# Kernel tuning notes

Measured on AMD Instinct MI355X. Metric: run time of the kernel, lower is better.

## Reference

```python
import jax, jax.numpy as jnp
import numpy as np

EPS = 1e-5

def _layer_norm(x, gamma, beta):
    mu = jnp.mean(x, axis=-1, keepdims=True)
    var = jnp.mean(jnp.square(x - mu), axis=-1, keepdims=True)
    return (x - mu) * jax.lax.rsqrt(var + EPS) * gamma + beta

def setup_inputs() -> dict:
    key = jax.random.key(0)
    ks = jax.random.split(key, 16)
    B, N, E, D = 1024, 64, 1024, 512
    s_e = 1.0 / np.sqrt(E)
    s_d = 1.0 / np.sqrt(D)
    return {
        "role_embeddings": jax.random.normal(ks[0], (B, N, E), jnp.float32),
        "context": jax.random.normal(ks[1], (B, D), jnp.float32),
        "qW": jax.random.uniform(ks[2], (E, E), jnp.float32, -s_e, s_e),
        "qb": jax.random.uniform(ks[3], (E,), jnp.float32, -s_e, s_e),
        "kW": jax.random.uniform(ks[4], (E, D), jnp.float32, -s_d, s_d),
        "kb": jax.random.uniform(ks[5], (E,), jnp.float32, -s_d, s_d),
        "vW": jax.random.uniform(ks[6], (E, D), jnp.float32, -s_d, s_d),
        "vb": jax.random.uniform(ks[7], (E,), jnp.float32, -s_d, s_d),
        "oW": jax.random.uniform(ks[8], (E, E), jnp.float32, -s_e, s_e),
        "ob": jax.random.uniform(ks[9], (E,), jnp.float32, -s_e, s_e),
        "lnq_g": jnp.ones((E,), jnp.float32),
        "lnq_b": jnp.zeros((E,), jnp.float32),
        "lnk_g": jnp.ones((D,), jnp.float32),
        "lnk_b": jnp.zeros((D,), jnp.float32),
    }

def reference(role_embeddings, context, qW, qb, kW, kb, vW, vb, oW, ob, lnq_g, lnq_b, lnk_g, lnk_b):
    E = role_embeddings.shape[-1]
    ctx = context[:, None, :]                                   # [B, 1, D]
    q = _layer_norm(role_embeddings, lnq_g, lnq_b) @ qW.T + qb  # [B, N, E]
    nk = _layer_norm(ctx, lnk_g, lnk_b)                         # [B, 1, D]
    k = nk @ kW.T + kb                                          # [B, 1, E]
    v = nk @ vW.T + vb                                          # [B, 1, E]
    scale = E ** (-0.5)
    scores = jnp.einsum('bne,bke->bnk', q, k) * scale           # [B, N, 1]
    attn = jnp.tanh(scores)
    out = attn * v                                              # broadcast -> [B, N, E]
    return (out + role_embeddings) @ oW.T + ob
```

## Files before the change

kernel.cpp:

```cpp
#include <hip/hip_runtime.h>

#define E_DIM 1024
#define D_DIM 512
#define B_DIM 1024
#define N_SEQ 64
#define M_ROWS (B_DIM * N_SEQ)

typedef __attribute__((ext_vector_type(8))) short bf16x8;
typedef __attribute__((ext_vector_type(4))) float f32x4;
typedef __attribute__((ext_vector_type(8))) unsigned short u16x8;

__device__ __forceinline__ float bf2f(unsigned short b) {
    union { unsigned int u; float f; } v; v.u = ((unsigned int)b) << 16; return v.f;
}
__device__ __forceinline__ unsigned short f2bf(float f) {
    union { float f; unsigned int u; } v; v.f = f;
    unsigned int r = v.u + 0x7FFFu + ((v.u >> 16) & 1u);
    return (unsigned short)(r >> 16);
}
__device__ __forceinline__ bool detect_bf16(const void* det) {
    return *(const unsigned int*)det == 0x3F803F80u;
}
__device__ __forceinline__ void load8(const void* p, size_t idx, bool isbf, float o[8]) {
    if (isbf) {
        const u16x8 v = *(const u16x8*)((const unsigned short*)p + idx);
#pragma unroll
        for (int j = 0; j < 8; j++) o[j] = bf2f(v[j]);
    } else {
        const float4 a = *(const float4*)((const float*)p + idx);
        const float4 b = *(const float4*)((const float*)p + idx + 4);
        o[0]=a.x; o[1]=a.y; o[2]=a.z; o[3]=a.w; o[4]=b.x; o[5]=b.y; o[6]=b.z; o[7]=b.w;
    }
}
__device__ __forceinline__ float load1(const void* p, size_t idx, bool isbf) {
    return isbf ? bf2f(((const unsigned short*)p)[idx]) : ((const float*)p)[idx];
}
__device__ __forceinline__ void gload16(const void* g, void* l) {
    __builtin_amdgcn_global_load_lds((const __attribute__((address_space(1))) void*)g,
                                     (__attribute__((address_space(3))) void*)l, 16, 0, 0);
}

__device__ __forceinline__ void block_reduce_2(float& s, float& s2, float* smem) {
#pragma unroll
    for (int off = 32; off; off >>= 1) {
        s  += __shfl_xor(s,  off, 64);
        s2 += __shfl_xor(s2, off, 64);
    }
    const int wave = threadIdx.x >> 6, lane = threadIdx.x & 63;
    if (lane == 0) { smem[wave * 2] = s; smem[wave * 2 + 1] = s2; }
    __syncthreads();
    s  = smem[0] + smem[2] + smem[4] + smem[6];
    s2 = smem[1] + smem[3] + smem[5] + smem[7];
}
__device__ __forceinline__ void block_reduce_3(float& a, float& b, float& c, float* smem) {
#pragma unroll
    for (int off = 32; off; off >>= 1) {
        a += __shfl_xor(a, off, 64);
        b += __shfl_xor(b, off, 64);
        c += __shfl_xor(c, off, 64);
    }
    const int wave = threadIdx.x >> 6, lane = threadIdx.x & 63;
    if (lane == 0) { smem[wave * 3] = a; smem[wave * 3 + 1] = b; smem[wave * 3 + 2] = c; }
    __syncthreads();
    a = smem[0] + smem[3] + smem[6] + smem[9];
    b = smem[1] + smem[4] + smem[7] + smem[10];
    c = smem[2] + smem[5] + smem[8] + smem[11];
}

__global__ void ctxln_k(const void* __restrict__ ctx, const void* __restrict__ g,
                        const void* __restrict__ bta, const void* __restrict__ det,
                        float* __restrict__ nk) {
    __shared__ float sm[8];
    const bool isbf = detect_bf16(det);
    const size_t base = (size_t)blockIdx.x * D_DIM;
    const int t = threadIdx.x;
    const float x0 = load1(ctx, base + t * 2, isbf);
    const float x1 = load1(ctx, base + t * 2 + 1, isbf);
    float s = x0 + x1, s2 = x0 * x0 + x1 * x1;
    block_reduce_2(s, s2, sm);
    const float m = s * (1.f / D_DIM);
    const float rs = rsqrtf(s2 * (1.f / D_DIM) - m * m + 1e-5f);
    nk[base + t * 2]     = (x0 - m) * rs * load1(g, t * 2, isbf)     + load1(bta, t * 2, isbf);
    nk[base + t * 2 + 1] = (x1 - m) * rs * load1(g, t * 2 + 1, isbf) + load1(bta, t * 2 + 1, isbf);
}

__global__ void transpose_k(const void* __restrict__ Win, const void* __restrict__ det,
                            float* __restrict__ out) {
    __shared__ float tile[32][33];
    const bool isbf = detect_bf16(det);
    const int bx = blockIdx.x * 32, by = blockIdx.y * 32;
    const int tx = threadIdx.x & 31, ty4 = (threadIdx.x >> 5) * 4;
#pragma unroll
    for (int i = 0; i < 4; i++)
        tile[ty4 + i][tx] = load1(Win, (size_t)(by + ty4 + i) * E_DIM + bx + tx, isbf);
    __syncthreads();
#pragma unroll
    for (int i = 0; i < 4; i++)
        out[(size_t)(bx + ty4 + i) * E_DIM + by + tx] = tile[tx][ty4 + i];
}

__global__ void castw_k(const void* __restrict__ Win, const void* __restrict__ det,
                        unsigned short* __restrict__ out, int n) {
    const bool isbf = detect_bf16(det);
    const int i = (blockIdx.x * 256 + threadIdx.x) * 8;
    if (i >= n) return;
    float a8[8];
    load8(Win, (size_t)i, isbf, a8);
    u16x8 h;
#pragma unroll
    for (int j = 0; j < 8; j++) h[j] = f2bf(a8[j]);
    *(u16x8*)(out + i) = h;
}

template <bool FORCEF32, int KDIM>
__launch_bounds__(256)
__global__ void sgemm_k(const float* __restrict__ A, const void* __restrict__ W,
                        const void* __restrict__ bias, float* __restrict__ C,
                        const void* __restrict__ det, int Ncols) {
    __shared__ __align__(16) unsigned short As[64][40];
    __shared__ __align__(16) unsigned short Bs[64][40];
    const bool isbf = FORCEF32 ? false : detect_bf16(det);
    const int tid = threadIdx.x;
    const int tileM = blockIdx.y * 64;
    const int tileN = blockIdx.x * 64;
    const int r = tid >> 2;
    const int cseg = (tid & 3) * 8;
    const int gm = tileM + r;
    const int gn = tileN + r;
    const int lane = tid & 63;
    const int wave = tid >> 6;
    const int quad = lane >> 4;
    const int l16 = lane & 15;

    f32x4 acc[4];
#pragma unroll
    for (int i = 0; i < 4; i++) acc[i] = (f32x4){0.f, 0.f, 0.f, 0.f};

    for (int k0 = 0; k0 < KDIM; k0 += 32) {
        const int gk = k0 + cseg;
        float a8[8], w8[8];
        load8(A, (size_t)gm * KDIM + gk, false, a8);
        load8(W, (size_t)gn * KDIM + gk, isbf, w8);
        __syncthreads();
#pragma unroll
        for (int j = 0; j < 8; j++) {
            As[r][cseg + j] = f2bf(a8[j]);
            Bs[r][cseg + j] = f2bf(w8[j]);
        }
        __syncthreads();
        const bf16x8 a = *(const bf16x8*)&As[wave * 16 + l16][quad * 8];
#pragma unroll
        for (int nt = 0; nt < 4; nt++) {
            const bf16x8 b = *(const bf16x8*)&Bs[nt * 16 + l16][quad * 8];
            acc[nt] = __builtin_amdgcn_mfma_f32_16x16x32_bf16(a, b, acc[nt], 0, 0, 0);
        }
    }
#pragma unroll
    for (int nt = 0; nt < 4; nt++) {
        const int gc = tileN + nt * 16 + l16;
        const float bv = bias ? load1(bias, gc, isbf) : 0.f;
#pragma unroll
        for (int rg = 0; rg < 4; rg++) {
            const int grow = tileM + wave * 16 + quad * 4 + rg;
            C[(size_t)grow * Ncols + gc] = acc[nt][rg] + bv;
        }
    }
}

__global__ void prep_k(const float* __restrict__ kvec, const float* __restrict__ kk,
                       const void* __restrict__ qb, const void* __restrict__ g,
                       const void* __restrict__ bta, const void* __restrict__ det,
                       float* __restrict__ gk, float* __restrict__ S1, float* __restrict__ C0) {
    __shared__ float sm[12];
    const bool isbf = detect_bf16(det);
    const size_t base = (size_t)blockIdx.x * E_DIM;
    const int t = threadIdx.x;
    float c = 0.f, s1 = 0.f, s2 = 0.f;
#pragma unroll
    for (int j = 0; j < 4; j++) {
        const int idx = t * 4 + j;
        const float kv = kvec[base + idx], kkv = kk[base + idx];
        const float gv = load1(g, idx, isbf);
        c  += load1(qb, idx, isbf) * kv;
        s1 += gv * kkv;
        s2 += load1(bta, idx, isbf) * kkv;
        gk[base + idx] = gv * kkv;
    }
    block_reduce_3(c, s1, s2, sm);
    if (t == 0) { S1[blockIdx.x] = s1; C0[blockIdx.x] = s2 + c; }
}

__global__ void rowscore_k(const void* __restrict__ role, const void* __restrict__ det,
                           const float* __restrict__ gk, const float* __restrict__ S1,
                           const float* __restrict__ C0, float* __restrict__ attn) {
    __shared__ float sm[12];
    const bool isbf = detect_bf16(det);
    const size_t m = blockIdx.x;
    const int b = (int)(m >> 6);
    const size_t base = m * E_DIM;
    const int t = threadIdx.x;
    float x[4];
    if (isbf) {
        const uint2 u = *(const uint2*)((const unsigned short*)role + base + t * 4);
        x[0] = bf2f(u.x & 0xFFFF); x[1] = bf2f(u.x >> 16);
        x[2] = bf2f(u.y & 0xFFFF); x[3] = bf2f(u.y >> 16);
    } else {
        const float4 v = *(const float4*)((const float*)role + base + t * 4);
        x[0]=v.x; x[1]=v.y; x[2]=v.z; x[3]=v.w;
    }
    const float4 gv = *(const float4*)(gk + ((size_t)b << 10) + t * 4);
    float s = 0.f, s2 = 0.f, d = 0.f;
    s = x[0]+x[1]+x[2]+x[3];
    s2 = x[0]*x[0]+x[1]*x[1]+x[2]*x[2]+x[3]*x[3];
    d = x[0]*gv.x + x[1]*gv.y + x[2]*gv.z + x[3]*gv.w;
    block_reduce_3(s, s2, d, sm);
    if (t == 0) {
        const float mu = s * (1.f / E_DIM);
        const float rstd = rsqrtf(s2 * (1.f / E_DIM) - mu * mu + 1e-5f);
        const float score = rstd * (d - mu * S1[b]) + C0[b];
        attn[m] = tanhf(score * 0.03125f);
    }
}

__launch_bounds__(256)
__global__ void outgemm_k(const void* __restrict__ role, const unsigned short* __restrict__ oWb,
                          const float* __restrict__ attn, const float* __restrict__ vo,
                          const void* __restrict__ ob, void* __restrict__ out,
                          const void* __restrict__ det) {
    __shared__ __align__(16) unsigned short As[128 * 32];
    __shared__ __align__(16) unsigned short Bs[128 * 32];
    const bool isbf = detect_bf16(det);
    const int tid = threadIdx.x;
    const int wave = tid >> 6, lane = tid & 63;
    const int quad = lane >> 4, l16 = lane & 15;
    const int wm = wave >> 1, wn = wave & 1;

    const int id = blockIdx.x + (blockIdx.y << 3);
    const int sid = (id & 7) * 512 + (id >> 3);
    const int tileN = (sid & 7) * 128;
    const int tileM = (sid >> 3) * 128;

    const int srow = lane >> 2;
    const int scol = (lane & 3) * 8;
    const int ar = tid >> 2;
    const int ac = (tid & 3) * 8;

    f32x4 acc[4][4];
#pragma unroll
    for (int i = 0; i < 4; i++)
#pragma unroll
        for (int j = 0; j < 4; j++) acc[i][j] = (f32x4){0.f, 0.f, 0.f, 0.f};

    const float* rolef = (const float*)role;
    const unsigned short* roleh = (const unsigned short*)role;

    for (int k0 = 0; k0 < E_DIM; k0 += 32) {
        __syncthreads();
#pragma unroll
        for (int c = 0; c < 2; c++) {
            const int cb = c * 4 + wave;
            const unsigned short* gp = oWb + (size_t)(tileN + cb * 16 + srow) * E_DIM + k0 + scol;
            gload16(gp, Bs + cb * 512);
        }
        if (isbf) {
#pragma unroll
            for (int c = 0; c < 2; c++) {
                const int cb = c * 4 + wave;
                const unsigned short* gp = roleh + (size_t)(tileM + cb * 16 + srow) * E_DIM + k0 + scol;
                gload16(gp, As + cb * 512);
            }
        } else {
#pragma unroll
            for (int c = 0; c < 2; c++) {
                const int rr = c * 64 + ar;
                const float* gp = rolef + (size_t)(tileM + rr) * E_DIM + k0 + ac;
                const float4 f0 = ((const float4*)gp)[0];
                const float4 f1 = ((const float4*)gp)[1];
                u16x8 h;
                h[0]=f2bf(f0.x); h[1]=f2bf(f0.y); h[2]=f2bf(f0.z); h[3]=f2bf(f0.w);
                h[4]=f2bf(f1.x); h[5]=f2bf(f1.y); h[6]=f2bf(f1.z); h[7]=f2bf(f1.w);
                *(u16x8*)(As + rr * 32 + ac) = h;
            }
        }
        __syncthreads();
        bf16x8 af[4], bfr[4];
#pragma unroll
        for (int mt = 0; mt < 4; mt++)
            af[mt] = *(const bf16x8*)(As + (wm * 64 + mt * 16 + l16) * 32 + quad * 8);
#pragma unroll
        for (int nt = 0; nt < 4; nt++)
            bfr[nt] = *(const bf16x8*)(Bs + (wn * 64 + nt * 16 + l16) * 32 + quad * 8);
#pragma unroll
        for (int mt = 0; mt < 4; mt++)
#pragma unroll
            for (int nt = 0; nt < 4; nt++)
                acc[mt][nt] = __builtin_amdgcn_mfma_f32_16x16x32_bf16(af[mt], bfr[nt], acc[mt][nt], 0, 0, 0);
    }
    const int b = (tileM >> 6) + wm;
#pragma unroll
    for (int nt = 0; nt < 4; nt++) {
        const int gc = tileN + wn * 64 + nt * 16 + l16;
        const float bv = load1(ob, gc, isbf);
        const float vv = vo[((size_t)b << 10) + gc];
#pragma unroll
        for (int mt = 0; mt < 4; mt++) {
#pragma unroll
            for (int rg = 0; rg < 4; rg++) {
                const int grow = tileM + wm * 64 + mt * 16 + quad * 4 + rg;
                const float val = acc[mt][nt][rg] + attn[grow] * vv + bv;
                const size_t off = (size_t)grow * E_DIM + gc;
                if (isbf) ((unsigned short*)out)[off] = f2bf(val);
                else      ((float*)out)[off] = val;
            }
        }
    }
}

extern "C" void kernel_launch(void* const* d_in, const int* in_sizes, int n_in,
                              void* d_out, int out_size, void* d_ws, size_t ws_size,
                              hipStream_t stream) {
    const void* role  = d_in[0];
    const void* ctx   = d_in[1];
    const void* qW    = d_in[2];
    const void* qb    = d_in[3];
    const void* kW    = d_in[4];
    const void* kb    = d_in[5];
    const void* vW    = d_in[6];
    const void* vb    = d_in[7];
    const void* oW    = d_in[8];
    const void* ob    = d_in[9];
    const void* lnq_g = d_in[10];
    const void* lnq_b = d_in[11];
    const void* lnk_g = d_in[12];
    const void* lnk_b = d_in[13];

    float* ws    = (float*)d_ws;
    float* kvec  = ws;
    float* vvec  = kvec + (1 << 20);
    float* slotA = vvec + (1 << 20);
    float* slotB = slotA + (1 << 20);
    float* gk    = slotB + (1 << 20);
    float* attn  = gk + (1 << 20);
    float* S1    = attn + (1 << 16);
    float* C0    = S1 + 1024;

    float* nk = slotA;
    ctxln_k<<<B_DIM, 256, 0, stream>>>(ctx, lnk_g, lnk_b, lnq_g, nk);
    dim3 g16(16, 16);
    sgemm_k<false, D_DIM><<<g16, 256, 0, stream>>>(nk, kW, kb, kvec, lnq_g, E_DIM);
    sgemm_k<false, D_DIM><<<g16, 256, 0, stream>>>(nk, vW, vb, vvec, lnq_g, E_DIM);
    float* qWT = slotA;
    transpose_k<<<dim3(32, 32), 256, 0, stream>>>(qW, lnq_g, qWT);
    float* kk = slotB;
    sgemm_k<true, E_DIM><<<g16, 256, 0, stream>>>(kvec, qWT, nullptr, kk, lnq_g, E_DIM);
    prep_k<<<B_DIM, 256, 0, stream>>>(kvec, kk, qb, lnq_g, lnq_b, lnq_g, gk, S1, C0);
    rowscore_k<<<M_ROWS, 256, 0, stream>>>(role, lnq_g, gk, S1, C0, attn);
    float* vo = slotB;
    sgemm_k<false, E_DIM><<<g16, 256, 0, stream>>>(vvec, oW, nullptr, vo, lnq_g, E_DIM);
    unsigned short* oWb = (unsigned short*)slotA;
    castw_k<<<512, 256, 0, stream>>>(oW, lnq_g, oWb, E_DIM * E_DIM);
    outgemm_k<<<dim3(8, 512), 256, 0, stream>>>(role, oWb, attn, vo, ob, d_out, lnq_g);
}
```

Before: 909.6 us.

## Merge small GEMMs, use wave-per-row scoring that writes bf16 role copy for output GEMM

Pairs of independent small GEMMs (k/v projections, and kk/vo) now run in single launches that select their operands by block index. The row-score kernel becomes one wave per row in a grid-stride loop with shuffle reductions instead of a 256-thread block per row. When the input is fp32 and the workspace is large enough, it also writes a bf16 copy of role_embeddings. The output GEMM then loads that copy with direct 16-byte loads instead of converting fp32 inside its main loop, at the cost of an extra 128MB write and read.

```diff
diff --git a/kernel.cpp b/kernel.cpp
--- a/kernel.cpp
+++ b/kernel.cpp
@@ -9,6 +9,7 @@
 typedef __attribute__((ext_vector_type(8))) short bf16x8;
 typedef __attribute__((ext_vector_type(4))) float f32x4;
 typedef __attribute__((ext_vector_type(8))) unsigned short u16x8;
+typedef __attribute__((ext_vector_type(4))) unsigned short u16x4;
 
 __device__ __forceinline__ float bf2f(unsigned short b) {
     union { unsigned int u; float f; } v; v.u = ((unsigned int)b) << 16; return v.f;
@@ -112,17 +113,24 @@
     *(u16x8*)(out + i) = h;
 }
 
-template <bool FORCEF32, int KDIM>
+template <int KDIM>
 __launch_bounds__(256)
-__global__ void sgemm_k(const float* __restrict__ A, const void* __restrict__ W,
-                        const void* __restrict__ bias, float* __restrict__ C,
-                        const void* __restrict__ det, int Ncols) {
+__global__ void sgemm2_k(const float* __restrict__ A0, const void* __restrict__ W0,
+                         const void* __restrict__ b0, float* __restrict__ C0_,
+                         const float* __restrict__ A1, const void* __restrict__ W1,
+                         const void* __restrict__ b1, float* __restrict__ C1_,
+                         const void* __restrict__ det, int w0f32, int w1f32) {
     __shared__ __align__(16) unsigned short As[64][40];
     __shared__ __align__(16) unsigned short Bs[64][40];
-    const bool isbf = FORCEF32 ? false : detect_bf16(det);
+    const bool sel = blockIdx.x >= 16;
+    const float* A = sel ? A1 : A0;
+    const void* W = sel ? W1 : W0;
+    const void* bias = sel ? b1 : b0;
+    float* C = sel ? C1_ : C0_;
+    const bool wbf = (sel ? w1f32 : w0f32) ? false : detect_bf16(det);
     const int tid = threadIdx.x;
     const int tileM = blockIdx.y * 64;
-    const int tileN = blockIdx.x * 64;
+    const int tileN = (blockIdx.x & 15) * 64;
     const int r = tid >> 2;
     const int cseg = (tid & 3) * 8;
     const int gm = tileM + r;
@@ -140,7 +148,7 @@
         const int gk = k0 + cseg;
         float a8[8], w8[8];
         load8(A, (size_t)gm * KDIM + gk, false, a8);
-        load8(W, (size_t)gn * KDIM + gk, isbf, w8);
+        load8(W, (size_t)gn * KDIM + gk, wbf, w8);
         __syncthreads();
 #pragma unroll
         for (int j = 0; j < 8; j++) {
@@ -158,19 +166,19 @@
 #pragma unroll
     for (int nt = 0; nt < 4; nt++) {
         const int gc = tileN + nt * 16 + l16;
-        const float bv = bias ? load1(bias, gc, isbf) : 0.f;
+        const float bv = bias ? load1(bias, gc, detect_bf16(det)) : 0.f;
 #pragma unroll
         for (int rg = 0; rg < 4; rg++) {
             const int grow = tileM + wave * 16 + quad * 4 + rg;
-            C[(size_t)grow * Ncols + gc] = acc[nt][rg] + bv;
-        }
-    }
-}
-
-__global__ void prep_k(const float* __restrict__ kvec, const float* __restrict__ kk,
+            C[(size_t)grow * E_DIM + gc] = acc[nt][rg] + bv;
+        }
+    }
+}
+
+__global__ void prep_k(const float* __restrict__ kvec, float* __restrict__ kkgk,
                        const void* __restrict__ qb, const void* __restrict__ g,
                        const void* __restrict__ bta, const void* __restrict__ det,
-                       float* __restrict__ gk, float* __restrict__ S1, float* __restrict__ C0) {
+                       float* __restrict__ S1, float* __restrict__ C0) {
     __shared__ float sm[12];
     const bool isbf = detect_bf16(det);
     const size_t base = (size_t)blockIdx.x * E_DIM;
@@ -179,12 +187,12 @@
 #pragma unroll
     for (int j = 0; j < 4; j++) {
         const int idx = t * 4 + j;
-        const float kv = kvec[base + idx], kkv = kk[base + idx];
+        const float kv = kvec[base + idx], kkv = kkgk[base + idx];
         const float gv = load1(g, idx, isbf);
         c  += load1(qb, idx, isbf) * kv;
         s1 += gv * kkv;
         s2 += load1(bta, idx, isbf) * kkv;
-        gk[base + idx] = gv * kkv;
+        kkgk[base + idx] = gv * kkv;
     }
     block_reduce_3(c, s1, s2, sm);
     if (t == 0) { S1[blockIdx.x] = s1; C0[blockIdx.x] = s2 + c; }
@@ -192,44 +200,75 @@
 
 __global__ void rowscore_k(const void* __restrict__ role, const void* __restrict__ det,
                            const float* __restrict__ gk, const float* __restrict__ S1,
-                           const float* __restrict__ C0, float* __restrict__ attn) {
-    __shared__ float sm[12];
-    const bool isbf = detect_bf16(det);
-    const size_t m = blockIdx.x;
-    const int b = (int)(m >> 6);
-    const size_t base = m * E_DIM;
-    const int t = threadIdx.x;
-    float x[4];
-    if (isbf) {
-        const uint2 u = *(const uint2*)((const unsigned short*)role + base + t * 4);
-        x[0] = bf2f(u.x & 0xFFFF); x[1] = bf2f(u.x >> 16);
-        x[2] = bf2f(u.y & 0xFFFF); x[3] = bf2f(u.y >> 16);
-    } else {
-        const float4 v = *(const float4*)((const float*)role + base + t * 4);
-        x[0]=v.x; x[1]=v.y; x[2]=v.z; x[3]=v.w;
-    }
-    const float4 gv = *(const float4*)(gk + ((size_t)b << 10) + t * 4);
-    float s = 0.f, s2 = 0.f, d = 0.f;
-    s = x[0]+x[1]+x[2]+x[3];
-    s2 = x[0]*x[0]+x[1]*x[1]+x[2]*x[2]+x[3]*x[3];
-    d = x[0]*gv.x + x[1]*gv.y + x[2]*gv.z + x[3]*gv.w;
-    block_reduce_3(s, s2, d, sm);
-    if (t == 0) {
-        const float mu = s * (1.f / E_DIM);
-        const float rstd = rsqrtf(s2 * (1.f / E_DIM) - mu * mu + 1e-5f);
-        const float score = rstd * (d - mu * S1[b]) + C0[b];
-        attn[m] = tanhf(score * 0.03125f);
+                           const float* __restrict__ C0, float* __restrict__ attn,
+                           unsigned short* __restrict__ roleb) {
+    const bool isbf = detect_bf16(det);
+    const int lane = threadIdx.x & 63;
+    const int gw = blockIdx.x * 4 + (threadIdx.x >> 6);
+    const int nw = gridDim.x * 4;
+    const bool wb = (!isbf) && (roleb != nullptr);
+    for (int m = gw; m < M_ROWS; m += nw) {
+        const int b = m >> 6;
+        const size_t base = (size_t)m * E_DIM;
+        const float* gkb = gk + ((size_t)b << 10);
+        float s = 0.f, s2 = 0.f, d = 0.f;
+        if (isbf) {
+            const unsigned short* rp = (const unsigned short*)role + base;
+#pragma unroll
+            for (int j = 0; j < 2; j++) {
+                const int col = lane * 8 + j * 512;
+                const u16x8 v = *(const u16x8*)(rp + col);
+                const float4 g0 = *(const float4*)(gkb + col);
+                const float4 g1 = *(const float4*)(gkb + col + 4);
+                float x[8];
+#pragma unroll
+                for (int i = 0; i < 8; i++) x[i] = bf2f(v[i]);
+#pragma unroll
+                for (int i = 0; i < 8; i++) { s += x[i]; s2 += x[i] * x[i]; }
+                d += x[0]*g0.x + x[1]*g0.y + x[2]*g0.z + x[3]*g0.w
+                   + x[4]*g1.x + x[5]*g1.y + x[6]*g1.z + x[7]*g1.w;
+            }
+        } else {
+            const float* rp = (const float*)role + base;
+#pragma unroll
+            for (int j = 0; j < 4; j++) {
+                const int col = lane * 4 + j * 256;
+                const float4 x = *(const float4*)(rp + col);
+                const float4 g = *(const float4*)(gkb + col);
+                s  += x.x + x.y + x.z + x.w;
+                s2 += x.x*x.x + x.y*x.y + x.z*x.z + x.w*x.w;
+                d  += x.x*g.x + x.y*g.y + x.z*g.z + x.w*g.w;
+                if (wb) {
+                    u16x4 h; h[0]=f2bf(x.x); h[1]=f2bf(x.y); h[2]=f2bf(x.z); h[3]=f2bf(x.w);
+                    *(u16x4*)(roleb + base + col) = h;
+                }
+            }
+        }
+#pragma unroll
+        for (int off = 32; off; off >>= 1) {
+            s  += __shfl_xor(s,  off, 64);
+            s2 += __shfl_xor(s2, off, 64);
+            d  += __shfl_xor(d,  off, 64);
+        }
+        if (lane == 0) {
+            const float mu = s * (1.f / E_DIM);
+            const float rstd = rsqrtf(s2 * (1.f / E_DIM) - mu * mu + 1e-5f);
+            attn[m] = tanhf((rstd * (d - mu * S1[b]) + C0[b]) * 0.03125f);
+        }
     }
 }
 
 __launch_bounds__(256)
-__global__ void outgemm_k(const void* __restrict__ role, const unsigned short* __restrict__ oWb,
+__global__ void outgemm_k(const void* __restrict__ role, const unsigned short* __restrict__ roleb,
+                          const unsigned short* __restrict__ oWb,
                           const float* __restrict__ attn, const float* __restrict__ vo,
                           const void* __restrict__ ob, void* __restrict__ out,
                           const void* __restrict__ det) {
     __shared__ __align__(16) unsigned short As[128 * 32];
     __shared__ __align__(16) unsigned short Bs[128 * 32];
     const bool isbf = detect_bf16(det);
+    const bool abf = isbf || (roleb != nullptr);
+    const unsigned short* Ab = isbf ? (const unsigned short*)role : roleb;
     const int tid = threadIdx.x;
     const int wave = tid >> 6, lane = tid & 63;
     const int quad = lane >> 4, l16 = lane & 15;
@@ -252,7 +291,6 @@
         for (int j = 0; j < 4; j++) acc[i][j] = (f32x4){0.f, 0.f, 0.f, 0.f};
 
     const float* rolef = (const float*)role;
-    const unsigned short* roleh = (const unsigned short*)role;
 
     for (int k0 = 0; k0 < E_DIM; k0 += 32) {
         __syncthreads();
@@ -262,11 +300,11 @@
             const unsigned short* gp = oWb + (size_t)(tileN + cb * 16 + srow) * E_DIM + k0 + scol;
             gload16(gp, Bs + cb * 512);
         }
-        if (isbf) {
+        if (abf) {
 #pragma unroll
             for (int c = 0; c < 2; c++) {
                 const int cb = c * 4 + wave;
-                const unsigned short* gp = roleh + (size_t)(tileM + cb * 16 + srow) * E_DIM + k0 + scol;
+                const unsigned short* gp = Ab + (size_t)(tileM + cb * 16 + srow) * E_DIM + k0 + scol;
                 gload16(gp, As + cb * 512);
             }
         } else {
@@ -297,6 +335,12 @@
                 acc[mt][nt] = __builtin_amdgcn_mfma_f32_16x16x32_bf16(af[mt], bfr[nt], acc[mt][nt], 0, 0, 0);
     }
     const int b = (tileM >> 6) + wm;
+    float at[4][4];
+#pragma unroll
+    for (int mt = 0; mt < 4; mt++)
+#pragma unroll
+        for (int rg = 0; rg < 4; rg++)
+            at[mt][rg] = attn[tileM + wm * 64 + mt * 16 + quad * 4 + rg];
 #pragma unroll
     for (int nt = 0; nt < 4; nt++) {
         const int gc = tileN + wn * 64 + nt * 16 + l16;
@@ -307,7 +351,7 @@
 #pragma unroll
             for (int rg = 0; rg < 4; rg++) {
                 const int grow = tileM + wm * 64 + mt * 16 + quad * 4 + rg;
-                const float val = acc[mt][nt][rg] + attn[grow] * vv + bv;
+                const float val = acc[mt][nt][rg] + at[mt][rg] * vv + bv;
                 const size_t off = (size_t)grow * E_DIM + gc;
                 if (isbf) ((unsigned short*)out)[off] = f2bf(val);
                 else      ((float*)out)[off] = val;
@@ -338,26 +382,28 @@
     float* kvec  = ws;
     float* vvec  = kvec + (1 << 20);
     float* slotA = vvec + (1 << 20);
-    float* slotB = slotA + (1 << 20);
-    float* gk    = slotB + (1 << 20);
-    float* attn  = gk + (1 << 20);
+    float* kkgk  = slotA + (1 << 20);
+    float* vo    = kkgk + (1 << 20);
+    float* attn  = vo + (1 << 20);
     float* S1    = attn + (1 << 16);
     float* C0    = S1 + 1024;
+    float* wend  = C0 + 1024;
+    const size_t used = (size_t)(wend - ws) * 4;
+    unsigned short* roleb = nullptr;
+    if (ws_size >= used + (size_t)M_ROWS * E_DIM * 2)
+        roleb = (unsigned short*)wend;
 
     float* nk = slotA;
     ctxln_k<<<B_DIM, 256, 0, stream>>>(ctx, lnk_g, lnk_b, lnq_g, nk);
-    dim3 g16(16, 16);
-    sgemm_k<false, D_DIM><<<g16, 256, 0, stream>>>(nk, kW, kb, kvec, lnq_g, E_DIM);
-    sgemm_k<false, D_DIM><<<g16, 256, 0, stream>>>(nk, vW, vb, vvec, lnq_g, E_DIM);
+    sgemm2_k<D_DIM><<<dim3(32, 16), 256, 0, stream>>>(
+        nk, kW, kb, kvec, nk, vW, vb, vvec, lnq_g, 0, 0);
     float* qWT = slotA;
     transpose_k<<<dim3(32, 32), 256, 0, stream>>>(qW, lnq_g, qWT);
-    float* kk = slotB;
-    sgemm_k<true, E_DIM><<<g16, 256, 0, stream>>>(kvec, qWT, nullptr, kk, lnq_g, E_DIM);
-    prep_k<<<B_DIM, 256, 0, stream>>>(kvec, kk, qb, lnq_g, lnq_b, lnq_g, gk, S1, C0);
-    rowscore_k<<<M_ROWS, 256, 0, stream>>>(role, lnq_g, gk, S1, C0, attn);
-    float* vo = slotB;
-    sgemm_k<false, E_DIM><<<g16, 256, 0, stream>>>(vvec, oW, nullptr, vo, lnq_g, E_DIM);
+    sgemm2_k<E_DIM><<<dim3(32, 16), 256, 0, stream>>>(
+        kvec, qWT, nullptr, kkgk, vvec, oW, nullptr, vo, lnq_g, 1, 0);
+    prep_k<<<B_DIM, 256, 0, stream>>>(kvec, kkgk, qb, lnq_g, lnq_b, lnq_g, S1, C0);
     unsigned short* oWb = (unsigned short*)slotA;
     castw_k<<<512, 256, 0, stream>>>(oW, lnq_g, oWb, E_DIM * E_DIM);
-    outgemm_k<<<dim3(8, 512), 256, 0, stream>>>(role, oWb, attn, vo, ob, d_out, lnq_g);
-}
+    rowscore_k<<<2048, 256, 0, stream>>>(role, lnq_g, kkgk, S1, C0, attn, roleb);
+    outgemm_k<<<dim3(8, 512), 256, 0, stream>>>(role, roleb, oWb, attn, vo, ob, d_out, lnq_g);
+}
```

Measured after the change: 804.0 us. 1.13x faster.
